# Kernel tuning notes

Hardware: AMD Instinct MI355X
Metric: run time of the kernel (lower is better)

Reference implementation:

```python
import jax, jax.numpy as jnp
import numpy as np

BS, SEQ_Q = 16, 2048
ATTN_DIM, K_DIM, HEAD, RANK = 1024, 1024, 16, 16
A_H = ATTN_DIM // HEAD        # 64
K_R = K_DIM // RANK           # 64
HR = HEAD * RANK              # 256
EXP = 2
EPS = 1e-5


def setup_inputs() -> dict:
    key = jax.random.key(0)
    ks = jax.random.split(key, 12)
    n = lambda k, shape, scale=1.0: jax.random.normal(k, shape, dtype=jnp.float32) * scale
    lin = ATTN_DIM ** -0.5
    xav = (2.0 / (K_R + RANK)) ** 0.5  # xavier_normal for factor
    return {
        "Q": n(ks[0], (BS, SEQ_Q, ATTN_DIM)),
        "K": n(ks[1], (BS, K_DIM, ATTN_DIM)),
        "V": n(ks[2], (BS, K_DIM, ATTN_DIM)),
        "WQ": n(ks[3], (ATTN_DIM, ATTN_DIM), lin), "bQ": jnp.zeros((ATTN_DIM,), jnp.float32),
        "WK": n(ks[4], (ATTN_DIM, ATTN_DIM), lin), "bK": jnp.zeros((ATTN_DIM,), jnp.float32),
        "WV": n(ks[5], (ATTN_DIM, ATTN_DIM), lin), "bV": jnp.zeros((ATTN_DIM,), jnp.float32),
        "factor": n(ks[6], (1, A_H, K_R, RANK), xav),
        "W1": n(ks[7], (EXP * ATTN_DIM, ATTN_DIM), lin), "b1": jnp.zeros((EXP * ATTN_DIM,), jnp.float32),
        "W2": n(ks[8], (ATTN_DIM, EXP * ATTN_DIM), (EXP * ATTN_DIM) ** -0.5), "b2": jnp.zeros((ATTN_DIM,), jnp.float32),
        "gamma": jnp.ones((ATTN_DIM,), jnp.float32),
        "beta": jnp.zeros((ATTN_DIM,), jnp.float32),
    }


def reference(Q, K, V, WQ, bQ, WK, bK, WV, bV, factor, W1, b1, W2, b2, gamma, beta):
    bs = Q.shape[0]
    fac = factor[0]  # [a_h, k_r, rank]
    # Q path: [bs, a_h, head*rank, seq_q/rank]
    q = (Q @ WQ.T + bQ).reshape(bs, A_H, HR, -1)
    # K/V path: low-rank projection via learned factor -> [bs, a_h, head*rank, rank]
    k = jnp.einsum('bahk,akr->bahr', (K @ WK.T + bK).reshape(bs, A_H, HR, K_R), fac)
    v = jnp.einsum('bahk,akr->bahr', (V @ WV.T + bV).reshape(bs, A_H, HR, K_R), fac)
    # scores: Q^T K / sqrt(head*rank) -> [bs, a_h, L, rank]
    scores = jnp.einsum('bahl,bahr->balr', q, k) / jnp.float32(HR) ** 0.5
    attn = jax.nn.softmax(scores, axis=-1)
    # attn @ V^T -> [bs, a_h, L, head*rank], then flatten back to [bs, seq_q, attn_dim]
    ctx = jnp.einsum('balr,bahr->balh', attn, v).reshape(bs, -1, ATTN_DIM)
    # FFN (dropout = identity in eval)
    h = jax.nn.relu(ctx @ W1.T + b1)
    y = h @ W2.T + b2
    # residual + LayerNorm
    x = y + Q
    mu = jnp.mean(x, axis=-1, keepdims=True)
    var = jnp.var(x, axis=-1, keepdims=True)
    return (x - mu) * jax.lax.rsqrt(var + EPS) * gamma + beta
```

## Files before the change

### kernel.cpp

```cpp
#include <hip/hip_runtime.h>
#include <cstdint>

typedef unsigned short u16;
typedef unsigned int   u32;
typedef u16    u16x4  __attribute__((ext_vector_type(4)));
typedef u16    u16x8  __attribute__((ext_vector_type(8)));
typedef __bf16 bf16x8 __attribute__((ext_vector_type(8)));
typedef float  f32x4  __attribute__((ext_vector_type(4)));

template<int N> struct IC { static constexpr int v = N; };

__device__ __forceinline__ u16 f2b(float x) {
  u32 u = __builtin_bit_cast(u32, x);
  u32 r = (u + 0x7fffu + ((u >> 16) & 1u)) >> 16;
  return (u16)r;
}
__device__ __forceinline__ float b2f(u16 u) {
  return __builtin_bit_cast(float, (u32)u << 16);
}

__device__ __forceinline__ void gl2lds16(const u16* g, u16* l) {
  __builtin_amdgcn_global_load_lds(
      (__attribute__((address_space(1))) void*)g,
      (__attribute__((address_space(3))) void*)l, 16, 0, 0);
}

struct CvtArgs {
  const float* src[8];
  u16*         dst[8];
  long         end[8];
};

__global__ __launch_bounds__(256) void cvt_all(CvtArgs a)
{
  long g = (long)blockIdx.x * 1024;
  int seg = 0;
#pragma unroll
  for (int s = 0; s < 8; ++s) seg += (g >= a.end[s]) ? 1 : 0;
  long base = (seg == 0) ? 0 : a.end[seg - 1];
  long off = g - base + (long)threadIdx.x * 4;
  const float* src = a.src[seg];
  u16* dst = a.dst[seg];
  f32x4 v = *(const f32x4*)&src[off];
  u16x4 o = { f2b(v[0]), f2b(v[1]), f2b(v[2]), f2b(v[3]) };
  *(u16x4*)&dst[off] = o;
}

__global__ __launch_bounds__(512, 2) void gemm256(
    const u16* __restrict__ A, const u16* __restrict__ B,
    const float* __restrict__ bias, u16* __restrict__ C,
    int M, int N, int K, int relu)
{
  __shared__ __attribute__((aligned(16))) u16 Abuf[2][16384];
  __shared__ __attribute__((aligned(16))) u16 Bbuf[2][16384];

  const int tid  = threadIdx.x;
  const int lane = tid & 63;
  const int wave = tid >> 6;
  const int lr   = lane & 15;
  const int quad = lane >> 4;
  const int wr   = wave >> 2;
  const int wc   = wave & 3;

  const int Nb = gridDim.x;
  const int flat = blockIdx.y * Nb + blockIdx.x;
  const int sg  = flat / (8 * Nb);
  const int rem = flat - sg * 8 * Nb;
  const int bx  = rem >> 3;
  const int by  = sg * 8 + (rem & 7);
  const long m0 = (long)by * 256;
  const long n0 = (long)bx * 256;

  long goff[2]; int loff[2];
#pragma unroll
  for (int c = 0; c < 2; ++c) {
    const int p = tid + 512 * c;
    const int row = p >> 3;
    const int logcol = (p & 7) ^ (row & 7);
    goff[c] = (long)row * K + logcol * 8;
    loff[c] = p * 8;
  }

  const u16* Ag = A + m0 * K;
  const u16* Bg = B + n0 * K;

  const int ph_0 = quad ^ (lane & 7);
  const int ph_1 = (quad + 4) ^ (lane & 7);

  f32x4 acc[8][4] = {};

  auto stage = [&](u16* lds, const u16* g, int h) {
#pragma unroll
    for (int c = 0; c < 2; ++c)
      gl2lds16(g + (long)h * 128 * K + goff[c], lds + h * 8192 + loff[c]);
  };
  auto ldA = [&](const u16* Ac, int i, int kk) -> bf16x8 {
    return *(const bf16x8*)&Ac[(wr * 128 + i * 16 + lr) * 64 + (kk ? ph_1 : ph_0) * 8];
  };
  auto ldB = [&](const u16* Bc, int j, int kk) -> bf16x8 {
    return *(const bf16x8*)&Bc[(wc * 64 + j * 16 + lr) * 64 + (kk ? ph_1 : ph_0) * 8];
  };

  auto ktile = [&](auto sa, auto sb, auto vm, const u16* Ac, const u16* Bc,
                   u16* Ast, u16* Bst, const u16* gAn, const u16* gBn) {
    bf16x8 afA[4][2], afB[4][2], bf0[2][2], bf1[2][2];
#pragma unroll
    for (int i = 0; i < 4; ++i) { afA[i][0] = ldA(Ac, i, 0); afA[i][1] = ldA(Ac, i, 1); }
#pragma unroll
    for (int j = 0; j < 2; ++j) { bf0[j][0] = ldB(Bc, j, 0); bf0[j][1] = ldB(Bc, j, 1); }
#pragma unroll
    for (int j = 0; j < 2; ++j) { bf1[j][0] = ldB(Bc, 2 + j, 0); bf1[j][1] = ldB(Bc, 2 + j, 1); }
#pragma unroll
    for (int i = 0; i < 4; ++i) { afB[i][0] = ldA(Ac, 4 + i, 0); afB[i][1] = ldA(Ac, 4 + i, 1); }
    __builtin_amdgcn_sched_barrier(0);
    if constexpr (decltype(sa)::v) stage(Ast, gAn, 0);
    __builtin_amdgcn_s_barrier();
    __builtin_amdgcn_s_setprio(1);
#pragma unroll
    for (int i = 0; i < 4; ++i)
#pragma unroll
      for (int j = 0; j < 2; ++j) {
        acc[i][j] = __builtin_amdgcn_mfma_f32_16x16x32_bf16(afA[i][0], bf0[j][0], acc[i][j], 0, 0, 0);
        acc[i][j] = __builtin_amdgcn_mfma_f32_16x16x32_bf16(afA[i][1], bf0[j][1], acc[i][j], 0, 0, 0);
      }
    __builtin_amdgcn_s_setprio(0);
    __builtin_amdgcn_s_barrier();
    if constexpr (decltype(sa)::v) stage(Ast, gAn, 1);
    __builtin_amdgcn_s_barrier();
    __builtin_amdgcn_s_setprio(1);
#pragma unroll
    for (int i = 0; i < 4; ++i)
#pragma unroll
      for (int j = 0; j < 2; ++j) {
        acc[i][2 + j] = __builtin_amdgcn_mfma_f32_16x16x32_bf16(afA[i][0], bf1[j][0], acc[i][2 + j], 0, 0, 0);
        acc[i][2 + j] = __builtin_amdgcn_mfma_f32_16x16x32_bf16(afA[i][1], bf1[j][1], acc[i][2 + j], 0, 0, 0);
      }
    __builtin_amdgcn_s_setprio(0);
    __builtin_amdgcn_s_barrier();
    if constexpr (decltype(sb)::v) stage(Bst, gBn, 0);
    __builtin_amdgcn_s_barrier();
    __builtin_amdgcn_s_setprio(1);
#pragma unroll
    for (int i = 0; i < 4; ++i)
#pragma unroll
      for (int j = 0; j < 2; ++j) {
        acc[4 + i][j] = __builtin_amdgcn_mfma_f32_16x16x32_bf16(afB[i][0], bf0[j][0], acc[4 + i][j], 0, 0, 0);
        acc[4 + i][j] = __builtin_amdgcn_mfma_f32_16x16x32_bf16(afB[i][1], bf0[j][1], acc[4 + i][j], 0, 0, 0);
      }
    __builtin_amdgcn_s_setprio(0);
    __builtin_amdgcn_s_barrier();
    if constexpr (decltype(sb)::v) stage(Bst, gBn, 1);
    __builtin_amdgcn_s_barrier();
    __builtin_amdgcn_s_setprio(1);
#pragma unroll
    for (int i = 0; i < 4; ++i)
#pragma unroll
      for (int j = 0; j < 2; ++j) {
        acc[4 + i][2 + j] = __builtin_amdgcn_mfma_f32_16x16x32_bf16(afB[i][0], bf1[j][0], acc[4 + i][2 + j], 0, 0, 0);
        acc[4 + i][2 + j] = __builtin_amdgcn_mfma_f32_16x16x32_bf16(afB[i][1], bf1[j][1], acc[4 + i][2 + j], 0, 0, 0);
      }
    __builtin_amdgcn_s_setprio(0);
    if constexpr (decltype(vm)::v == 4) asm volatile("s_waitcnt vmcnt(4)" ::: "memory");
    if constexpr (decltype(vm)::v == 0) asm volatile("s_waitcnt vmcnt(0)" ::: "memory");
    __builtin_amdgcn_s_barrier();
  };

  const int NT = K >> 6;

  stage(&Abuf[0][0], Ag, 0); stage(&Abuf[0][0], Ag, 1);
  stage(&Bbuf[0][0], Bg, 0); stage(&Bbuf[0][0], Bg, 1);
  stage(&Bbuf[1][0], Bg + 64, 0); stage(&Bbuf[1][0], Bg + 64, 1);
  asm volatile("s_waitcnt vmcnt(4)" ::: "memory");
  __builtin_amdgcn_s_barrier();

  for (int t = 0; t < NT - 2; ++t) {
    const int cur = t & 1, nxt = cur ^ 1;
    ktile(IC<1>{}, IC<1>{}, IC<4>{},
          &Abuf[cur][0], &Bbuf[cur][0],
          &Abuf[nxt][0], &Bbuf[cur][0],
          Ag + (long)(t + 1) * 64, Bg + (long)(t + 2) * 64);
  }
  {
    const int cur = (NT - 2) & 1, nxt = cur ^ 1;
    ktile(IC<1>{}, IC<0>{}, IC<0>{},
          &Abuf[cur][0], &Bbuf[cur][0],
          &Abuf[nxt][0], nullptr,
          Ag + (long)(NT - 1) * 64, nullptr);
  }
  {
    const int cur = (NT - 1) & 1;
    ktile(IC<0>{}, IC<0>{}, IC<-1>{},
          &Abuf[cur][0], &Bbuf[cur][0],
          nullptr, nullptr, nullptr, nullptr);
  }

#pragma unroll
  for (int j = 0; j < 4; ++j) {
    const int col = wc * 64 + j * 16 + lr;
    const float bv = bias[n0 + col];
#pragma unroll
    for (int i = 0; i < 8; ++i) {
#pragma unroll
      for (int r = 0; r < 4; ++r) {
        const int row = wr * 128 + i * 16 + quad * 4 + r;
        float v = acc[i][j][r] + bv;
        if (relu) v = fmaxf(v, 0.0f);
        C[(m0 + row) * (long)N + (n0 + col)] = f2b(v);
      }
    }
  }
}

__global__ __launch_bounds__(256) void attn_kernel(
    const u16* __restrict__ Qp, const u16* __restrict__ Kp,
    const u16* __restrict__ Vp, const float* __restrict__ factor,
    u16* __restrict__ Ctx)
{
  __shared__ __attribute__((aligned(16))) float fac_s[64 * 16];
  __shared__ __attribute__((aligned(16))) float k_s[256][20];
  __shared__ __attribute__((aligned(16))) float v_s[256][20];
  __shared__ __attribute__((aligned(16))) float s_s[128][20];

  const int t = threadIdx.x;
  const int b = blockIdx.x >> 6;
  const int a = blockIdx.x & 63;

  for (int i = t; i < 1024; i += 256) fac_s[i] = factor[a * 1024 + i];
  __syncthreads();

  {
    const long kb = (((long)(b * 1024 + a * 16)) << 10) + (long)t * 64;
    float kacc[16] = {}, vacc[16] = {};
    for (int kk8 = 0; kk8 < 64; kk8 += 8) {
      u16x8 kv8 = *(const u16x8*)&Kp[kb + kk8];
      u16x8 vv8 = *(const u16x8*)&Vp[kb + kk8];
#pragma unroll
      for (int j = 0; j < 8; ++j) {
        const float kv = b2f(kv8[j]), vv = b2f(vv8[j]);
        const float* fr = &fac_s[(kk8 + j) * 16];
#pragma unroll
        for (int r = 0; r < 16; ++r) { kacc[r] += kv * fr[r]; vacc[r] += vv * fr[r]; }
      }
    }
#pragma unroll
    for (int r = 0; r < 16; ++r) { k_s[t][r] = kacc[r] * 0.0625f; v_s[t][r] = vacc[r]; }
  }
  __syncthreads();

  {
    const int l = t & 127, half = t >> 7;
    const long qb = (((long)(b * 2048 + a * 32)) << 10) + l;
    f32x4 acc0 = {}, acc1 = {};
    for (int h = 0; h < 256; ++h) {
      const float qv = b2f(Qp[qb + (long)h * 128]);
      f32x4 k0 = *(const f32x4*)&k_s[h][half * 8];
      f32x4 k1 = *(const f32x4*)&k_s[h][half * 8 + 4];
      acc0 += k0 * qv;
      acc1 += k1 * qv;
    }
    *(f32x4*)&s_s[l][half * 8]     = acc0;
    *(f32x4*)&s_s[l][half * 8 + 4] = acc1;
  }
  __syncthreads();

  if (t < 128) {
    float vals[16];
    float m = -1e30f;
#pragma unroll
    for (int r = 0; r < 16; ++r) { vals[r] = s_s[t][r]; m = fmaxf(m, vals[r]); }
    float sum = 0.0f;
#pragma unroll
    for (int r = 0; r < 16; ++r) { vals[r] = __expf(vals[r] - m); sum += vals[r]; }
    const float inv = 1.0f / sum;
#pragma unroll
    for (int r = 0; r < 16; ++r) s_s[t][r] = vals[r] * inv;
  }
  __syncthreads();

  {
    f32x4 v0 = *(const f32x4*)&v_s[t][0];
    f32x4 v1 = *(const f32x4*)&v_s[t][4];
    f32x4 v2 = *(const f32x4*)&v_s[t][8];
    f32x4 v3 = *(const f32x4*)&v_s[t][12];
    const long cb = (((long)(b * 2048 + a * 32)) << 10) + t;
    for (int l = 0; l < 128; ++l) {
      f32x4 a0 = *(const f32x4*)&s_s[l][0];
      f32x4 a1 = *(const f32x4*)&s_s[l][4];
      f32x4 a2 = *(const f32x4*)&s_s[l][8];
      f32x4 a3 = *(const f32x4*)&s_s[l][12];
      f32x4 p = a0 * v0 + a1 * v1 + a2 * v2 + a3 * v3;
      Ctx[cb + (long)l * 256] = f2b(p[0] + p[1] + p[2] + p[3]);
    }
  }
}

__global__ __launch_bounds__(256) void ln_kernel(
    const u16* __restrict__ Y, const float* __restrict__ Qin,
    const float* __restrict__ gamma, const float* __restrict__ beta,
    float* __restrict__ out)
{
  const long row = blockIdx.x;
  const int t = threadIdx.x;
  const long base = (row << 10) + (long)t * 4;

  u16x4 y4 = *(const u16x4*)&Y[base];
  f32x4 q4 = *(const f32x4*)&Qin[base];
  f32x4 x;
#pragma unroll
  for (int c = 0; c < 4; ++c) x[c] = b2f(y4[c]) + q4[c];

  float s  = x[0] + x[1] + x[2] + x[3];
  float sq = x[0]*x[0] + x[1]*x[1] + x[2]*x[2] + x[3]*x[3];
#pragma unroll
  for (int o = 1; o < 64; o <<= 1) {
    s  += __shfl_xor(s, o);
    sq += __shfl_xor(sq, o);
  }
  __shared__ float red[8];
  if ((t & 63) == 0) { red[(t >> 6) * 2] = s; red[(t >> 6) * 2 + 1] = sq; }
  __syncthreads();
  s  = red[0] + red[2] + red[4] + red[6];
  sq = red[1] + red[3] + red[5] + red[7];

  const float mean = s * (1.0f / 1024.0f);
  const float var  = sq * (1.0f / 1024.0f) - mean * mean;
  const float rstd = rsqrtf(var + 1e-5f);

  f32x4 g4 = *(const f32x4*)&gamma[t * 4];
  f32x4 be4 = *(const f32x4*)&beta[t * 4];
  f32x4 o4;
#pragma unroll
  for (int c = 0; c < 4; ++c) o4[c] = (x[c] - mean) * rstd * g4[c] + be4[c];
  *(f32x4*)&out[base] = o4;
}

extern "C" void kernel_launch(void* const* d_in, const int* in_sizes, int n_in,
                              void* d_out, int out_size, void* d_ws, size_t ws_size,
                              hipStream_t stream)
{
  (void)in_sizes; (void)n_in; (void)out_size; (void)ws_size;
  const float* Q      = (const float*)d_in[0];
  const float* K      = (const float*)d_in[1];
  const float* V      = (const float*)d_in[2];
  const float* WQ     = (const float*)d_in[3];
  const float* bQ     = (const float*)d_in[4];
  const float* WK     = (const float*)d_in[5];
  const float* bK     = (const float*)d_in[6];
  const float* WV     = (const float*)d_in[7];
  const float* bV     = (const float*)d_in[8];
  const float* factor = (const float*)d_in[9];
  const float* W1     = (const float*)d_in[10];
  const float* b1     = (const float*)d_in[11];
  const float* W2     = (const float*)d_in[12];
  const float* b2     = (const float*)d_in[13];
  const float* gamma  = (const float*)d_in[14];
  const float* beta   = (const float*)d_in[15];
  float* out = (float*)d_out;

  const long NQ = 33554432L;
  const long NK = 16777216L;
  const long ND = 1048576L;
  const long NW = 2097152L;

  char* w = (char*)d_ws;
  u16* Qb  = (u16*)(w);
  u16* Kb  = (u16*)(w + 67108864L);
  u16* Vb  = (u16*)(w + 100663296L);
  u16* WQb = (u16*)(w + 134217728L);
  u16* WKb = (u16*)(w + 136314880L);
  u16* WVb = (u16*)(w + 138412032L);
  u16* W1b = (u16*)(w + 140509184L);
  u16* W2b = (u16*)(w + 144703488L);
  u16* Qp  = (u16*)(w + 148897792L);
  u16* Kp  = (u16*)(w + 216006656L);
  u16* Vp  = (u16*)(w + 249561088L);
  u16* Ctx = (u16*)(w + 283115520L);
  u16* Hb  = (u16*)(w);
  u16* Yb  = (u16*)(w + 216006656L);

  CvtArgs ca;
  ca.src[0] = Q;  ca.dst[0] = Qb;
  ca.src[1] = K;  ca.dst[1] = Kb;
  ca.src[2] = V;  ca.dst[2] = Vb;
  ca.src[3] = WQ; ca.dst[3] = WQb;
  ca.src[4] = WK; ca.dst[4] = WKb;
  ca.src[5] = WV; ca.dst[5] = WVb;
  ca.src[6] = W1; ca.dst[6] = W1b;
  ca.src[7] = W2; ca.dst[7] = W2b;
  long sizes[8] = { NQ, NK, NK, ND, ND, ND, NW, NW };
  long cum = 0;
  for (int i = 0; i < 8; ++i) { cum += sizes[i]; ca.end[i] = cum; }
  cvt_all<<<(int)(cum / 1024), 256, 0, stream>>>(ca);

  gemm256<<<dim3(4, 128), 512, 0, stream>>>(Qb, WQb, bQ, Qp, 32768, 1024, 1024, 0);
  gemm256<<<dim3(4, 64),  512, 0, stream>>>(Kb, WKb, bK, Kp, 16384, 1024, 1024, 0);
  gemm256<<<dim3(4, 64),  512, 0, stream>>>(Vb, WVb, bV, Vp, 16384, 1024, 1024, 0);

  attn_kernel<<<1024, 256, 0, stream>>>(Qp, Kp, Vp, factor, Ctx);

  gemm256<<<dim3(8, 128), 512, 0, stream>>>(Ctx, W1b, b1, Hb, 32768, 2048, 1024, 1);
  gemm256<<<dim3(4, 128), 512, 0, stream>>>(Hb, W2b, b2, Yb, 32768, 1024, 2048, 0);

  ln_kernel<<<32768, 256, 0, stream>>>(Yb, Q, gamma, beta, out);
}
```

Measured before the change: 954.5 us.

## Restructure GEMM k-loop to prefetch A and B two tiles ahead with fewer barriers

Reworks the software pipeline of the bf16 MFMA GEMM main loop. Both A and B are now prefetched two k-tiles ahead into the current buffer after all fragments are read, and the number of workgroup barriers per k-tile drops from about seven to two. MFMAs are regrouped so each k-half runs back to back across the tile, and the vmcnt wait is raised to allow more loads in flight. The cost is more outstanding memory traffic and a tighter dependence on the lgkmcnt wait to avoid overwriting LDS before every wave has read it.

```diff
diff --git a/kernel.cpp b/kernel.cpp
--- a/kernel.cpp
+++ b/kernel.cpp
@@ -101,8 +101,8 @@
     return *(const bf16x8*)&Bc[(wc * 64 + j * 16 + lr) * 64 + (kk ? ph_1 : ph_0) * 8];
   };
 
-  auto ktile = [&](auto sa, auto sb, auto vm, const u16* Ac, const u16* Bc,
-                   u16* Ast, u16* Bst, const u16* gAn, const u16* gBn) {
+  auto ktile = [&](auto st, auto vm, const u16* Ac, const u16* Bc,
+                   u16* Ast, u16* Bst, const u16* gA2, const u16* gB2) {
     bf16x8 afA[4][2], afB[4][2], bf0[2][2], bf1[2][2];
 #pragma unroll
     for (int i = 0; i < 4; ++i) { afA[i][0] = ldA(Ac, i, 0); afA[i][1] = ldA(Ac, i, 1); }
@@ -113,85 +113,74 @@
 #pragma unroll
     for (int i = 0; i < 4; ++i) { afB[i][0] = ldA(Ac, 4 + i, 0); afB[i][1] = ldA(Ac, 4 + i, 1); }
     __builtin_amdgcn_sched_barrier(0);
-    if constexpr (decltype(sa)::v) stage(Ast, gAn, 0);
+    __builtin_amdgcn_s_setprio(1);
+#pragma unroll
+    for (int kk = 0; kk < 2; ++kk)
+#pragma unroll
+      for (int i = 0; i < 4; ++i)
+#pragma unroll
+        for (int j = 0; j < 2; ++j)
+          acc[i][j] = __builtin_amdgcn_mfma_f32_16x16x32_bf16(afA[i][kk], bf0[j][kk], acc[i][j], 0, 0, 0);
+#pragma unroll
+    for (int kk = 0; kk < 2; ++kk)
+#pragma unroll
+      for (int i = 0; i < 4; ++i)
+#pragma unroll
+        for (int j = 0; j < 2; ++j)
+          acc[i][2 + j] = __builtin_amdgcn_mfma_f32_16x16x32_bf16(afA[i][kk], bf1[j][kk], acc[i][2 + j], 0, 0, 0);
+    __builtin_amdgcn_s_setprio(0);
+    asm volatile("s_waitcnt lgkmcnt(0)" ::: "memory");
     __builtin_amdgcn_s_barrier();
+    if constexpr (decltype(st)::v) { stage(Ast, gA2, 0); stage(Bst, gB2, 0); }
     __builtin_amdgcn_s_setprio(1);
 #pragma unroll
-    for (int i = 0; i < 4; ++i)
-#pragma unroll
-      for (int j = 0; j < 2; ++j) {
-        acc[i][j] = __builtin_amdgcn_mfma_f32_16x16x32_bf16(afA[i][0], bf0[j][0], acc[i][j], 0, 0, 0);
-        acc[i][j] = __builtin_amdgcn_mfma_f32_16x16x32_bf16(afA[i][1], bf0[j][1], acc[i][j], 0, 0, 0);
-      }
+    for (int kk = 0; kk < 2; ++kk)
+#pragma unroll
+      for (int i = 0; i < 4; ++i)
+#pragma unroll
+        for (int j = 0; j < 2; ++j)
+          acc[4 + i][j] = __builtin_amdgcn_mfma_f32_16x16x32_bf16(afB[i][kk], bf0[j][kk], acc[4 + i][j], 0, 0, 0);
     __builtin_amdgcn_s_setprio(0);
-    __builtin_amdgcn_s_barrier();
-    if constexpr (decltype(sa)::v) stage(Ast, gAn, 1);
-    __builtin_amdgcn_s_barrier();
+    if constexpr (decltype(st)::v) { stage(Ast, gA2, 1); stage(Bst, gB2, 1); }
     __builtin_amdgcn_s_setprio(1);
 #pragma unroll
-    for (int i = 0; i < 4; ++i)
-#pragma unroll
-      for (int j = 0; j < 2; ++j) {
-        acc[i][2 + j] = __builtin_amdgcn_mfma_f32_16x16x32_bf16(afA[i][0], bf1[j][0], acc[i][2 + j], 0, 0, 0);
-        acc[i][2 + j] = __builtin_amdgcn_mfma_f32_16x16x32_bf16(afA[i][1], bf1[j][1], acc[i][2 + j], 0, 0, 0);
-      }
+    for (int kk = 0; kk < 2; ++kk)
+#pragma unroll
+      for (int i = 0; i < 4; ++i)
+#pragma unroll
+        for (int j = 0; j < 2; ++j)
+          acc[4 + i][2 + j] = __builtin_amdgcn_mfma_f32_16x16x32_bf16(afB[i][kk], bf1[j][kk], acc[4 + i][2 + j], 0, 0, 0);
     __builtin_amdgcn_s_setprio(0);
-    __builtin_amdgcn_s_barrier();
-    if constexpr (decltype(sb)::v) stage(Bst, gBn, 0);
-    __builtin_amdgcn_s_barrier();
-    __builtin_amdgcn_s_setprio(1);
-#pragma unroll
-    for (int i = 0; i < 4; ++i)
-#pragma unroll
-      for (int j = 0; j < 2; ++j) {
-        acc[4 + i][j] = __builtin_amdgcn_mfma_f32_16x16x32_bf16(afB[i][0], bf0[j][0], acc[4 + i][j], 0, 0, 0);
-        acc[4 + i][j] = __builtin_amdgcn_mfma_f32_16x16x32_bf16(afB[i][1], bf0[j][1], acc[4 + i][j], 0, 0, 0);
-      }
-    __builtin_amdgcn_s_setprio(0);
-    __builtin_amdgcn_s_barrier();
-    if constexpr (decltype(sb)::v) stage(Bst, gBn, 1);
-    __builtin_amdgcn_s_barrier();
-    __builtin_amdgcn_s_setprio(1);
-#pragma unroll
-    for (int i = 0; i < 4; ++i)
-#pragma unroll
-      for (int j = 0; j < 2; ++j) {
-        acc[4 + i][2 + j] = __builtin_amdgcn_mfma_f32_16x16x32_bf16(afB[i][0], bf1[j][0], acc[4 + i][2 + j], 0, 0, 0);
-        acc[4 + i][2 + j] = __builtin_amdgcn_mfma_f32_16x16x32_bf16(afB[i][1], bf1[j][1], acc[4 + i][2 + j], 0, 0, 0);
-      }
-    __builtin_amdgcn_s_setprio(0);
-    if constexpr (decltype(vm)::v == 4) asm volatile("s_waitcnt vmcnt(4)" ::: "memory");
+    if constexpr (decltype(vm)::v == 8) asm volatile("s_waitcnt vmcnt(8)" ::: "memory");
     if constexpr (decltype(vm)::v == 0) asm volatile("s_waitcnt vmcnt(0)" ::: "memory");
     __builtin_amdgcn_s_barrier();
   };
 
   const int NT = K >> 6;
 
-  stage(&Abuf[0][0], Ag, 0); stage(&Abuf[0][0], Ag, 1);
-  stage(&Bbuf[0][0], Bg, 0); stage(&Bbuf[0][0], Bg, 1);
+  stage(&Abuf[0][0], Ag, 0);      stage(&Abuf[0][0], Ag, 1);
+  stage(&Bbuf[0][0], Bg, 0);      stage(&Bbuf[0][0], Bg, 1);
+  stage(&Abuf[1][0], Ag + 64, 0); stage(&Abuf[1][0], Ag + 64, 1);
   stage(&Bbuf[1][0], Bg + 64, 0); stage(&Bbuf[1][0], Bg + 64, 1);
-  asm volatile("s_waitcnt vmcnt(4)" ::: "memory");
+  asm volatile("s_waitcnt vmcnt(8)" ::: "memory");
   __builtin_amdgcn_s_barrier();
 
   for (int t = 0; t < NT - 2; ++t) {
-    const int cur = t & 1, nxt = cur ^ 1;
-    ktile(IC<1>{}, IC<1>{}, IC<4>{},
+    const int cur = t & 1;
+    ktile(IC<1>{}, IC<8>{},
           &Abuf[cur][0], &Bbuf[cur][0],
-          &Abuf[nxt][0], &Bbuf[cur][0],
-          Ag + (long)(t + 1) * 64, Bg + (long)(t + 2) * 64);
-  }
-  {
-    const int cur = (NT - 2) & 1, nxt = cur ^ 1;
-    ktile(IC<1>{}, IC<0>{}, IC<0>{},
           &Abuf[cur][0], &Bbuf[cur][0],
-          &Abuf[nxt][0], nullptr,
-          Ag + (long)(NT - 1) * 64, nullptr);
+          Ag + (long)(t + 2) * 64, Bg + (long)(t + 2) * 64);
+  }
+  {
+    const int cur = (NT - 2) & 1;
+    ktile(IC<0>{}, IC<0>{},
+          &Abuf[cur][0], &Bbuf[cur][0], nullptr, nullptr, nullptr, nullptr);
   }
   {
     const int cur = (NT - 1) & 1;
-    ktile(IC<0>{}, IC<0>{}, IC<-1>{},
-          &Abuf[cur][0], &Bbuf[cur][0],
-          nullptr, nullptr, nullptr, nullptr);
+    ktile(IC<0>{}, IC<-1>{},
+          &Abuf[cur][0], &Bbuf[cur][0], nullptr, nullptr, nullptr, nullptr);
   }
 
 #pragma unroll
```

Result: no change. 941.3 us (-1.4%).
